# Kernel optimization log

Measured on AMD Instinct MI355X. Metric: run time of the kernel, lower is better.

Reference implementation:

```python
import jax, jax.numpy as jnp
import numpy as np

B, N, INDIM = 512, 200, 200
D1, D2, D3 = 32, 32, 8
RATIO = 0.5
K1 = int(np.ceil(RATIO * N))    # 100 nodes kept after pool1
K2 = int(np.ceil(RATIO * K1))   # 50 nodes kept after pool2
BN_EPS = 1e-5
NEG = -1e9


def setup_inputs() -> dict:
    key = jax.random.key(0)
    ks = jax.random.split(key, 16)
    x = jax.random.normal(ks[0], (B, N, INDIM), jnp.float32)
    u = jax.random.uniform(ks[1], (B, N, N), jnp.float32)
    ut = jnp.triu(jnp.where(u > 0.9, u, 0.0), 1)
    adj = ut + jnp.swapaxes(ut, 1, 2)
    g = lambda i, shape: jax.random.normal(ks[i], shape, jnp.float32) * 0.1
    return dict(
        x=x, adj=adj,
        W1=g(2, (INDIM, D1)), a1s=g(3, (D1,)), a1d=g(4, (D1,)), b1=jnp.zeros((D1,), jnp.float32),
        W2=g(5, (D1, D2)), a2s=g(6, (D2,)), a2d=g(7, (D2,)), b2=jnp.zeros((D2,), jnp.float32),
        pw1=g(8, (D1,)), pw2=g(9, (D2,)),
        fc1_w=g(10, ((D1 + D2) * 2, D2)), fc1_b=jnp.zeros((D2,), jnp.float32),
        fc2_w=g(11, (D2, D3)), fc2_b=jnp.zeros((D3,), jnp.float32),
        fc3_w=g(12, (D3, 2)), fc3_b=jnp.zeros((2,), jnp.float32),
        bn4_g=jnp.ones((D2,), jnp.float32), bn4_b=jnp.zeros((D2,), jnp.float32),
        bn5_g=jnp.ones((D3,), jnp.float32), bn5_b=jnp.zeros((D3,), jnp.float32))


def _gat(x, mask, W, a_s, a_d, b):
    # PyG GATConv (heads=1): alpha_ij = softmax_j LeakyReLU(a_d.h_i + a_s.h_j) over in-neighbors j (self-loops added)
    h = jnp.einsum('bnf,fd->bnd', x, W)
    es = h @ a_s                    # [B,n] source term
    ed = h @ a_d                    # [B,n] dest term
    m = mask | jnp.eye(mask.shape[1], dtype=bool)
    logits = jax.nn.leaky_relu(ed[:, :, None] + es[:, None, :], 0.2)
    alpha = jax.nn.softmax(jnp.where(m, logits, NEG), axis=-1)   # [B,n,n]
    return jnp.einsum('bij,bjd->bid', alpha, h) + b


def _topk(x, adj_w, w, k):
    # TopKPooling(multiplier=1, nonlinearity=sigmoid): score = sigmoid(x.w/||w||)
    score = jax.nn.sigmoid((x @ w) / (jnp.linalg.norm(w) + 1e-16))   # [B,n]
    vals, idx = jax.lax.top_k(score, k)                              # perm sorted desc, as PyG
    xk = jnp.take_along_axis(x, idx[:, :, None], axis=1) * vals[:, :, None]
    ak = jnp.take_along_axis(jnp.take_along_axis(adj_w, idx[:, :, None], axis=1), idx[:, None, :], axis=2)
    return xk, ak, vals


def _bn(z, g, b):
    # eval-mode BatchNorm1d: running_mean=0, running_var=1
    return g * z / jnp.sqrt(1.0 + BN_EPS) + b


def reference(x, adj, W1, a1s, a1d, b1, W2, a2s, a2d, b2, pw1, pw2,
              fc1_w, fc1_b, fc2_w, fc2_b, fc3_w, fc3_b, bn4_g, bn4_b, bn5_g, bn5_b):
    h = _gat(x, adj > 0, W1, a1s, a1d, b1)
    h, aw, s1 = _topk(h, adj, pw1, K1)
    x1 = jnp.concatenate([h.max(axis=1), h.mean(axis=1)], axis=1)    # [B, 64]
    # augment_adj: add self-loops, spspmm (A+I)@(A+I), remove self-loops
    eye = jnp.eye(K1, dtype=aw.dtype)
    a2 = jnp.einsum('bij,bjk->bik', aw + eye, aw + eye) * (1.0 - eye)
    h = _gat(h, a2 != 0, W2, a2s, a2d, b2)
    h, _, s2 = _topk(h, a2, pw2, K2)
    x2 = jnp.concatenate([h.max(axis=1), h.mean(axis=1)], axis=1)    # [B, 64]
    z = jnp.concatenate([x1, x2], axis=1)                            # [B, 128]
    z = _bn(jax.nn.relu(z @ fc1_w + fc1_b), bn4_g, bn4_b)            # dropout: eval -> identity
    z = _bn(jax.nn.relu(z @ fc2_w + fc2_b), bn5_g, bn5_b)
    logp = jax.nn.log_softmax(z @ fc3_w + fc3_b, axis=-1)            # [B, 2]
    return logp, s1, s2
```

## Files before the change

kernel.cpp:

```cpp
#include <hip/hip_runtime.h>
#include <math.h>

#define N_    200
#define B_    512
#define K1_   100
#define K2_   50
#define ST    36
#define XS    21
#define KT    20
#define NT    10

#define S1_OFF 1024
#define S2_OFF 52224

__device__ __forceinline__ float lrelu(float v) { return v > 0.f ? v : 0.2f * v; }
__device__ __forceinline__ float sigm(float v)  { return 1.f / (1.f + __expf(-v)); }


__global__ __launch_bounds__(256) void gnn_fused(
    const float* __restrict__ x, const float* __restrict__ adj,
    const float* __restrict__ W1, const float* __restrict__ a1s,
    const float* __restrict__ a1d, const float* __restrict__ b1,
    const float* __restrict__ W2g, const float* __restrict__ a2s,
    const float* __restrict__ a2d, const float* __restrict__ b2,
    const float* __restrict__ pw1, const float* __restrict__ pw2,
    const float* __restrict__ fc1w, const float* __restrict__ fc1b,
    const float* __restrict__ fc2w, const float* __restrict__ fc2b,
    const float* __restrict__ fc3w, const float* __restrict__ fc3b,
    const float* __restrict__ bn4g, const float* __restrict__ bn4b,
    const float* __restrict__ bn5g, const float* __restrict__ bn5b,
    float* __restrict__ out)
{
  __shared__ __align__(16) char smem[72768];
  float*    sXs   = (float*)smem;
  float*    sW2   = (float*)smem;
  unsigned* sMask2= (unsigned*)(smem + 4096);
  float*    sH    = (float*)(smem + 33600);
  float*    sXK   = sH + 100 * ST;
  unsigned* sBITS = (unsigned*)(smem + 62400);
  float*    sES   = (float*)(smem + 68800);
  float*    sED   = (float*)(smem + 69600);
  float*    sKey  = (float*)(smem + 70400);
  int*      sSel  = (int*)(smem + 71424);
  float*    sVal  = (float*)(smem + 71824);
  float*    sXV   = (float*)(smem + 72224);
  float*    sRed  = (float*)(smem + 72736);

  const int t  = threadIdx.x;
  const int b  = blockIdx.x;
  const int wv = t >> 6, ln = t & 63;
  const float* xb = x   + (size_t)b * N_ * N_;
  const float* ab = adj + (size_t)b * N_ * N_;
  const float4* xb4 = (const float4*)xb;

  float acc[32];
  #pragma unroll
  for (int d = 0; d < 32; ++d) acc[d] = 0.f;

  float4 q0, q1, q2, q3;
  {
    int f0 = t,        r0 = f0 / 5, c0 = f0 % 5;
    int f1 = t + 256,  r1 = f1 / 5, c1 = f1 % 5;
    int f2 = t + 512,  r2 = f2 / 5, c2 = f2 % 5;
    int f3 = t + 768,  r3 = f3 / 5, c3 = f3 % 5;
    q0 = xb4[r0 * 50 + c0];
    q1 = xb4[r1 * 50 + c1];
    q2 = xb4[r2 * 50 + c2];
    if (f3 < 1000) q3 = xb4[r3 * 50 + c3];
    float* d0 = sXs + r0 * XS + c0 * 4; d0[0]=q0.x; d0[1]=q0.y; d0[2]=q0.z; d0[3]=q0.w;
    float* d1 = sXs + r1 * XS + c1 * 4; d1[0]=q1.x; d1[1]=q1.y; d1[2]=q1.z; d1[3]=q1.w;
    float* d2 = sXs + r2 * XS + c2 * 4; d2[0]=q2.x; d2[1]=q2.y; d2[2]=q2.z; d2[3]=q2.w;
    if (f3 < 1000) { float* d3 = sXs + r3 * XS + c3 * 4; d3[0]=q3.x; d3[1]=q3.y; d3[2]=q3.z; d3[3]=q3.w; }
  }
  __syncthreads();

  int cur = 0;
  for (int it = 0; it < NT; ++it) {
    if (it + 1 < NT) {
      int kb4 = (it + 1) * (KT / 4);
      int f0 = t,       r0 = f0 / 5, c0 = f0 % 5;
      int f1 = t + 256, r1 = f1 / 5, c1 = f1 % 5;
      int f2 = t + 512, r2 = f2 / 5, c2 = f2 % 5;
      int f3 = t + 768, r3 = f3 / 5, c3 = f3 % 5;
      q0 = xb4[r0 * 50 + kb4 + c0];
      q1 = xb4[r1 * 50 + kb4 + c1];
      q2 = xb4[r2 * 50 + kb4 + c2];
      if (f3 < 1000) q3 = xb4[r3 * 50 + kb4 + c3];
    }
    {
      int rbase = wv * 50 + it * 5;
      for (int rr = 0; rr < 5; ++rr) {
        int row = rbase + rr;
        const float* arow = ab + row * N_;
        float a0 = arow[ln];
        float a1 = arow[64 + ln];
        float a2 = arow[128 + ln];
        float a3 = (ln < 8) ? arow[192 + ln] : -1.f;
        unsigned long long b0 = __ballot(a0 > 0.f);
        unsigned long long b1 = __ballot(a1 > 0.f);
        unsigned long long b2 = __ballot(a2 > 0.f);
        unsigned long long b3 = __ballot(a3 > 0.f);
        if (ln == 0) {
          sBITS[row * 8 + 0] = (unsigned)b0; sBITS[row * 8 + 1] = (unsigned)(b0 >> 32);
          sBITS[row * 8 + 2] = (unsigned)b1; sBITS[row * 8 + 3] = (unsigned)(b1 >> 32);
          sBITS[row * 8 + 4] = (unsigned)b2; sBITS[row * 8 + 5] = (unsigned)(b2 >> 32);
          sBITS[row * 8 + 6] = (unsigned)b3;
        }
      }
    }
    if (t < N_) {
      const float* xr = sXs + cur * 4200 + t * XS;
      const int k0 = it * KT;
      for (int k = 0; k < KT; k += 4) {
        float x0 = xr[k], x1 = xr[k + 1], x2 = xr[k + 2], x3 = xr[k + 3];
        const float* w0 = W1 + (k0 + k) * 32;
        const float* w1 = w0 + 32;
        const float* w2 = w0 + 64;
        const float* w3 = w0 + 96;
        #pragma unroll
        for (int d = 0; d < 32; ++d) acc[d] += x0 * w0[d];
        #pragma unroll
        for (int d = 0; d < 32; ++d) acc[d] += x1 * w1[d];
        #pragma unroll
        for (int d = 0; d < 32; ++d) acc[d] += x2 * w2[d];
        #pragma unroll
        for (int d = 0; d < 32; ++d) acc[d] += x3 * w3[d];
      }
    }
    __syncthreads();
    if (it + 1 < NT) {
      float* B = sXs + (cur ^ 1) * 4200;
      int f0 = t,       r0 = f0 / 5, c0 = f0 % 5;
      int f1 = t + 256, r1 = f1 / 5, c1 = f1 % 5;
      int f2 = t + 512, r2 = f2 / 5, c2 = f2 % 5;
      int f3 = t + 768, r3 = f3 / 5, c3 = f3 % 5;
      float* d0 = B + r0 * XS + c0 * 4; d0[0]=q0.x; d0[1]=q0.y; d0[2]=q0.z; d0[3]=q0.w;
      float* d1 = B + r1 * XS + c1 * 4; d1[0]=q1.x; d1[1]=q1.y; d1[2]=q1.z; d1[3]=q1.w;
      float* d2 = B + r2 * XS + c2 * 4; d2[0]=q2.x; d2[1]=q2.y; d2[2]=q2.z; d2[3]=q2.w;
      if (f3 < 1000) { float* d3 = B + r3 * XS + c3 * 4; d3[0]=q3.x; d3[1]=q3.y; d3[2]=q3.z; d3[3]=q3.w; }
      __syncthreads();
    }
    cur ^= 1;
  }

  if (t < N_) {
    float es = 0.f, ed = 0.f;
    #pragma unroll
    for (int d = 0; d < 32; ++d) { es += acc[d] * a1s[d]; ed += acc[d] * a1d[d]; }
    sES[t] = es; sED[t] = ed;
    #pragma unroll
    for (int d = 0; d < 32; ++d) sH[t * ST + d] = acc[d];
  }
  __syncthreads();

  for (int i = t; i < 1024; i += 256) sW2[i] = W2g[i];
  {
    float v = (t < N_) ? sES[t] : -3.0e38f;
    #pragma unroll
    for (int off = 1; off < 64; off <<= 1) v = fmaxf(v, __shfl_xor(v, off, 64));
    if ((t & 63) == 0) sRed[t >> 6] = v;
  }
  __syncthreads();
  {
    float esmax = fmaxf(fmaxf(sRed[0], sRed[1]), fmaxf(sRed[2], sRed[3]));

    if (t < N_) {
      unsigned long long m0 = (unsigned long long)sBITS[t * 8 + 0] | ((unsigned long long)sBITS[t * 8 + 1] << 32);
      unsigned long long m1 = (unsigned long long)sBITS[t * 8 + 2] | ((unsigned long long)sBITS[t * 8 + 3] << 32);
      unsigned long long m2 = (unsigned long long)sBITS[t * 8 + 4] | ((unsigned long long)sBITS[t * 8 + 5] << 32);
      unsigned long long m3 = (unsigned long long)sBITS[t * 8 + 6];
      if (t < 64)       m0 |= 1ull << t;
      else if (t < 128) m1 |= 1ull << (t - 64);
      else if (t < 192) m2 |= 1ull << (t - 128);
      else              m3 |= 1ull << (t - 192);
      float ed_i = sED[t];
      float L = lrelu(ed_i + esmax);
      float ssum = 0.f;
      #pragma unroll
      for (int d = 0; d < 32; ++d) acc[d] = 0.f;
      #define AGG(mm, base)                                                        \
        while (mm) {                                                               \
          int j = (base) + (int)__builtin_ctzll(mm); mm &= (mm - 1);               \
          float w = __expf(lrelu(ed_i + sES[j]) - L); ssum += w;                   \
          const float* hr = &sH[j * ST];                                           \
          _Pragma("unroll")                                                        \
          for (int c = 0; c < 8; ++c) {                                            \
            float4 hv = *(const float4*)(hr + c * 4);                              \
            acc[c*4+0] += w * hv.x; acc[c*4+1] += w * hv.y;                        \
            acc[c*4+2] += w * hv.z; acc[c*4+3] += w * hv.w;                        \
          }                                                                        \
        }
      AGG(m0, 0) AGG(m1, 64) AGG(m2, 128) AGG(m3, 192)
      #undef AGG
      float inv = 1.f / ssum;
      #pragma unroll
      for (int d = 0; d < 32; ++d) acc[d] = acc[d] * inv + b1[d];
    }
    __syncthreads();
    if (t < N_) {
      #pragma unroll
      for (int d = 0; d < 32; ++d) sH[t * ST + d] = acc[d];
    }
  }
  __syncthreads();

  {
    float npw = 0.f;
    #pragma unroll
    for (int d = 0; d < 32; ++d) npw += pw1[d] * pw1[d];
    npw = sqrtf(npw) + 1e-16f;
    float sc = -1.f;
    if (t < N_) {
      float dp = 0.f;
      #pragma unroll
      for (int d = 0; d < 32; ++d) dp += sH[t * ST + d] * pw1[d];
      sc = sigm(dp / npw);
    }
    sKey[t] = sc;
  }
  __syncthreads();
  if (t < N_) {
    float sc = sKey[t];
    int rank = 0;
    for (int j = 0; j < N_; j += 4) {
      #pragma unroll
      for (int jj = 0; jj < 4; ++jj) {
        float o = sKey[j + jj];
        rank += (o > sc || (o == sc && (j + jj) < t)) ? 1 : 0;
      }
    }
    if (rank < K1_) {
      sSel[rank] = t; sVal[rank] = sc;
      out[S1_OFF + b * K1_ + rank] = sc;
    }
  }
  __syncthreads();
  {
    float tmp[13];
    #pragma unroll
    for (int it = 0; it < 13; ++it) {
      int i = t + it * 256;
      if (i < K1_ * 32) tmp[it] = sH[sSel[i >> 5] * ST + (i & 31)] * sVal[i >> 5];
    }
    __syncthreads();
    #pragma unroll
    for (int it = 0; it < 13; ++it) {
      int i = t + it * 256;
      if (i < K1_ * 32) sXK[(i >> 5) * ST + (i & 31)] = tmp[it];
    }
  }
  __syncthreads();
  if (t < 32) {
    float m = -3.0e38f, s = 0.f;
    for (int r = 0; r < K1_; ++r) { float v = sXK[r * ST + t]; m = fmaxf(m, v); s += v; }
    sXV[t] = m; sXV[32 + t] = s / 100.f;
  }

  if (t < K1_) {
    int gi = sSel[t];
    #pragma unroll
    for (int w = 0; w < 4; ++w) {
      unsigned m = 0;
      const int lim = (w < 3) ? 32 : 4;
      for (int jj = 0; jj < lim; ++jj) {
        int j = w * 32 + jj;
        int gj = sSel[j];
        unsigned bit = (sBITS[gi * 8 + (gj >> 5)] >> (gj & 31)) & 1u;
        if (j == t) bit = 1u;
        m |= bit << jj;
      }
      sMask2[t * 5 + w] = m;
    }
  }
  __syncthreads();
  {
    unsigned pr0 = 0, pr1 = 0, pr2 = 0, pr3 = 0;
    if (t < K1_) {
      #pragma unroll
      for (int kw = 0; kw < 4; ++kw) {
        unsigned mk = sMask2[t * 5 + kw];
        const int lim = (kw < 3) ? 32 : 4;
        for (int kk = 0; kk < lim; ++kk) {
          if ((mk >> kk) & 1u) {
            int k = kw * 32 + kk;
            pr0 |= sMask2[k * 5 + 0]; pr1 |= sMask2[k * 5 + 1];
            pr2 |= sMask2[k * 5 + 2]; pr3 |= sMask2[k * 5 + 3];
          }
        }
      }
    }
    __syncthreads();
    if (t < K1_) {
      sMask2[t * 5 + 0] = pr0; sMask2[t * 5 + 1] = pr1;
      sMask2[t * 5 + 2] = pr2; sMask2[t * 5 + 3] = pr3;
    }
  }
  __syncthreads();

  if (t < K1_) {
    float xk[32];
    #pragma unroll
    for (int c = 0; c < 8; ++c) *(float4*)&xk[c * 4] = *(const float4*)&sXK[t * ST + c * 4];
    float acc2[32];
    #pragma unroll
    for (int d = 0; d < 32; ++d) acc2[d] = 0.f;
    #pragma unroll
    for (int k = 0; k < 32; ++k) {
      float xv = xk[k];
      const float* wr = &sW2[k * 32];
      #pragma unroll
      for (int d = 0; d < 32; ++d) acc2[d] += xv * wr[d];
    }
    float es = 0.f, ed = 0.f;
    #pragma unroll
    for (int d = 0; d < 32; ++d) { es += acc2[d] * a2s[d]; ed += acc2[d] * a2d[d]; }
    sES[t] = es; sED[t] = ed;
    #pragma unroll
    for (int d = 0; d < 32; ++d) sH[t * ST + d] = acc2[d];
  }
  __syncthreads();
  {
    float v = (t < K1_) ? sES[t] : -3.0e38f;
    #pragma unroll
    for (int off = 1; off < 64; off <<= 1) v = fmaxf(v, __shfl_xor(v, off, 64));
    if ((t & 63) == 0) sRed[t >> 6] = v;
  }
  __syncthreads();
  {
    float esm2 = fmaxf(fmaxf(sRed[0], sRed[1]), fmaxf(sRed[2], sRed[3]));
    float acc2[32];
    if (t < K1_) {
      float ed_i = sED[t];
      float L = lrelu(ed_i + esm2);
      float ssum = 0.f;
      #pragma unroll
      for (int d = 0; d < 32; ++d) acc2[d] = 0.f;
      #pragma unroll
      for (int jw = 0; jw < 4; ++jw) {
        unsigned mw = sMask2[t * 5 + jw];
        const int lim = (jw < 3) ? 32 : 4;
        for (int jj = 0; jj < lim; ++jj) {
          int j = jw * 32 + jj;
          float w = 0.f;
          if ((mw >> jj) & 1u) w = __expf(lrelu(ed_i + sES[j]) - L);
          ssum += w;
          const float* hr = &sH[j * ST];
          #pragma unroll
          for (int d = 0; d < 32; ++d) acc2[d] += w * hr[d];
        }
      }
      float inv = 1.f / ssum;
      #pragma unroll
      for (int d = 0; d < 32; ++d) acc2[d] = acc2[d] * inv + b2[d];
    }
    __syncthreads();
    if (t < K1_) {
      #pragma unroll
      for (int d = 0; d < 32; ++d) sH[t * ST + d] = acc2[d];
    }
  }
  __syncthreads();

  {
    float npw = 0.f;
    #pragma unroll
    for (int d = 0; d < 32; ++d) npw += pw2[d] * pw2[d];
    npw = sqrtf(npw) + 1e-16f;
    if (t < K1_) {
      float dp = 0.f;
      #pragma unroll
      for (int d = 0; d < 32; ++d) dp += sH[t * ST + d] * pw2[d];
      sKey[t] = sigm(dp / npw);
    }
  }
  __syncthreads();
  if (t < K1_) {
    float sc = sKey[t];
    int rank = 0;
    for (int j = 0; j < K1_; j += 4) {
      #pragma unroll
      for (int jj = 0; jj < 4; ++jj) {
        float o = sKey[j + jj];
        rank += (o > sc || (o == sc && (j + jj) < t)) ? 1 : 0;
      }
    }
    if (rank < K2_) {
      sSel[rank] = t; sVal[rank] = sc;
      out[S2_OFF + b * K2_ + rank] = sc;
    }
  }
  __syncthreads();
  {
    int d = t & 31, r0 = t >> 5;
    for (int r = r0; r < K2_; r += 8) sXK[r * ST + d] = sH[sSel[r] * ST + d] * sVal[r];
  }
  __syncthreads();
  if (t < 32) {
    float m = -3.0e38f, s = 0.f;
    for (int r = 0; r < K2_; ++r) { float v = sXK[r * ST + t]; m = fmaxf(m, v); s += v; }
    sXV[64 + t] = m; sXV[96 + t] = s / 50.f;
  }
  __syncthreads();

  const float RS = 0.99999500003749969f;
  if (t < 32) {
    float z = fc1b[t];
    for (int k = 0; k < 128; ++k) z += sXV[k] * fc1w[k * 32 + t];
    z = fmaxf(z, 0.f);
    z = bn4g[t] * z * RS + bn4b[t];
    sKey[t] = z;
  }
  __syncthreads();
  if (t < 8) {
    float z = fc2b[t];
    for (int k = 0; k < 32; ++k) z += sKey[k] * fc2w[k * 8 + t];
    z = fmaxf(z, 0.f);
    z = bn5g[t] * z * RS + bn5b[t];
    sKey[32 + t] = z;
  }
  __syncthreads();
  if (t < 2) {
    float z = fc3b[t];
    for (int k = 0; k < 8; ++k) z += sKey[32 + k] * fc3w[k * 2 + t];
    sKey[40 + t] = z;
  }
  __syncthreads();
  if (t < 2) {
    float z0 = sKey[40], z1 = sKey[41];
    float m = fmaxf(z0, z1);
    float lse = m + logf(__expf(z0 - m) + __expf(z1 - m));
    out[b * 2 + t] = sKey[40 + t] - lse;
  }
}

extern "C" void kernel_launch(void* const* d_in, const int* in_sizes, int n_in,
                              void* d_out, int out_size, void* d_ws, size_t ws_size,
                              hipStream_t stream) {
  (void)in_sizes; (void)n_in; (void)d_ws; (void)ws_size; (void)out_size;
  const float* x    = (const float*)d_in[0];
  const float* adj  = (const float*)d_in[1];
  const float* W1   = (const float*)d_in[2];
  const float* a1s  = (const float*)d_in[3];
  const float* a1d  = (const float*)d_in[4];
  const float* b1   = (const float*)d_in[5];
  const float* W2   = (const float*)d_in[6];
  const float* a2s  = (const float*)d_in[7];
  const float* a2d  = (const float*)d_in[8];
  const float* b2   = (const float*)d_in[9];
  const float* pw1  = (const float*)d_in[10];
  const float* pw2  = (const float*)d_in[11];
  const float* fc1w = (const float*)d_in[12];
  const float* fc1b = (const float*)d_in[13];
  const float* fc2w = (const float*)d_in[14];
  const float* fc2b = (const float*)d_in[15];
  const float* fc3w = (const float*)d_in[16];
  const float* fc3b = (const float*)d_in[17];
  const float* bn4g = (const float*)d_in[18];
  const float* bn4b = (const float*)d_in[19];
  const float* bn5g = (const float*)d_in[20];
  const float* bn5b = (const float*)d_in[21];

  gnn_fused<<<B_, 256, 0, stream>>>(x, adj, W1, a1s, a1d, b1, W2, a2s, a2d, b2,
                                    pw1, pw2, fc1w, fc1b, fc2w, fc2b, fc3w, fc3b,
                                    bn4g, bn4b, bn5g, bn5b, (float*)d_out);
}
```

Baseline: 343.7 us.

## Split fused kernel into parallel projection/mask kernel and graph kernel

The first GAT projection (x@W1) and the adjacency-to-bitmask conversion move out of the single per-graph kernel into a separate kernel with four blocks per graph. That kernel splits nodes and output columns across blocks and waves and writes h and the mask bits to the workspace. The second kernel reloads them and runs the rest of the pipeline with a smaller shared-memory footprint, so more blocks fit per CU. The aim is more parallelism and occupancy for the memory-heavy first stage, at the cost of a global round trip for h and bits plus an extra launch.

```diff
diff --git a/kernel.cpp b/kernel.cpp
--- a/kernel.cpp
+++ b/kernel.cpp
@@ -6,23 +6,76 @@
 #define K1_   100
 #define K2_   50
 #define ST    36
-#define XS    21
-#define KT    20
-#define NT    10
 
 #define S1_OFF 1024
 #define S2_OFF 52224
 
+#define WS_BITS_OFF 13107200
+
 __device__ __forceinline__ float lrelu(float v) { return v > 0.f ? v : 0.2f * v; }
 __device__ __forceinline__ float sigm(float v)  { return 1.f / (1.f + __expf(-v)); }
 
-
-__global__ __launch_bounds__(256) void gnn_fused(
+__global__ __launch_bounds__(256) void gnn_k1(
     const float* __restrict__ x, const float* __restrict__ adj,
-    const float* __restrict__ W1, const float* __restrict__ a1s,
-    const float* __restrict__ a1d, const float* __restrict__ b1,
-    const float* __restrict__ W2g, const float* __restrict__ a2s,
-    const float* __restrict__ a2d, const float* __restrict__ b2,
+    const float* __restrict__ W1, float* __restrict__ gh,
+    unsigned* __restrict__ gbits)
+{
+  const int bid = blockIdx.x;
+  const int g = bid >> 2, c = bid & 3;
+  const int t = threadIdx.x;
+  const int wv = t >> 6, ln = t & 63;
+  const float* ag = adj + (size_t)g * N_ * N_;
+
+  for (int r = wv; r < 50; r += 4) {
+    int row = c * 50 + r;
+    const float* arow = ag + row * N_;
+    float a0 = arow[ln];
+    float a1 = arow[64 + ln];
+    float a2 = arow[128 + ln];
+    float a3 = (ln < 8) ? arow[192 + ln] : -1.f;
+    unsigned long long b0 = __ballot(a0 > 0.f);
+    unsigned long long b1 = __ballot(a1 > 0.f);
+    unsigned long long b2 = __ballot(a2 > 0.f);
+    unsigned long long b3 = __ballot(a3 > 0.f);
+    if (ln == 0) {
+      unsigned* bp = gbits + (size_t)(g * N_ + row) * 8;
+      *(uint4*)bp       = make_uint4((unsigned)b0, (unsigned)(b0 >> 32),
+                                     (unsigned)b1, (unsigned)(b1 >> 32));
+      *(uint4*)(bp + 4) = make_uint4((unsigned)b2, (unsigned)(b2 >> 32),
+                                     (unsigned)b3, 0u);
+    }
+  }
+
+  const int q = wv, n = t & 63;
+  if (n < 50) {
+    const int node = c * 50 + n;
+    const float* xr = x + (size_t)g * N_ * N_ + node * N_;
+    const float* Wq = W1 + q * 8;
+    float acc[8];
+    #pragma unroll
+    for (int d = 0; d < 8; ++d) acc[d] = 0.f;
+    for (int k = 0; k < N_; k += 4) {
+      float4 xv = *(const float4*)(xr + k);
+      #pragma unroll
+      for (int kk = 0; kk < 4; ++kk) {
+        float xs = (&xv.x)[kk];
+        const float* wr = Wq + (k + kk) * 32;
+        #pragma unroll
+        for (int d = 0; d < 8; ++d) acc[d] += xs * wr[d];
+      }
+    }
+    float* hp = gh + (size_t)(g * N_ + node) * 32 + q * 8;
+    *(float4*)hp       = make_float4(acc[0], acc[1], acc[2], acc[3]);
+    *(float4*)(hp + 4) = make_float4(acc[4], acc[5], acc[6], acc[7]);
+  }
+}
+
+__global__ __launch_bounds__(256) void gnn_k2(
+    const float* __restrict__ gh, const unsigned* __restrict__ gbits,
+    const float* __restrict__ a1s, const float* __restrict__ a1d,
+    const float* __restrict__ b1,  const float* __restrict__ W2g,
+    const float* __restrict__ a2s, const float* __restrict__ a2d,
+    const float* __restrict__ b2,
     const float* __restrict__ pw1, const float* __restrict__ pw2,
     const float* __restrict__ fc1w, const float* __restrict__ fc1b,
     const float* __restrict__ fc2w, const float* __restrict__ fc2b,
@@ -31,129 +84,56 @@
     const float* __restrict__ bn5g, const float* __restrict__ bn5b,
     float* __restrict__ out)
 {
-  __shared__ __align__(16) char smem[72768];
-  float*    sXs   = (float*)smem;
-  float*    sW2   = (float*)smem;
-  unsigned* sMask2= (unsigned*)(smem + 4096);
-  float*    sH    = (float*)(smem + 33600);
+  __shared__ __align__(16) char smem[45264];
+  float*    sH    = (float*)smem;
   float*    sXK   = sH + 100 * ST;
-  unsigned* sBITS = (unsigned*)(smem + 62400);
-  float*    sES   = (float*)(smem + 68800);
-  float*    sED   = (float*)(smem + 69600);
-  float*    sKey  = (float*)(smem + 70400);
-  int*      sSel  = (int*)(smem + 71424);
-  float*    sVal  = (float*)(smem + 71824);
-  float*    sXV   = (float*)(smem + 72224);
-  float*    sRed  = (float*)(smem + 72736);
-
-  const int t  = threadIdx.x;
-  const int b  = blockIdx.x;
-  const int wv = t >> 6, ln = t & 63;
-  const float* xb = x   + (size_t)b * N_ * N_;
-  const float* ab = adj + (size_t)b * N_ * N_;
-  const float4* xb4 = (const float4*)xb;
-
-  float acc[32];
-  #pragma unroll
-  for (int d = 0; d < 32; ++d) acc[d] = 0.f;
-
-  float4 q0, q1, q2, q3;
-  {
-    int f0 = t,        r0 = f0 / 5, c0 = f0 % 5;
-    int f1 = t + 256,  r1 = f1 / 5, c1 = f1 % 5;
-    int f2 = t + 512,  r2 = f2 / 5, c2 = f2 % 5;
-    int f3 = t + 768,  r3 = f3 / 5, c3 = f3 % 5;
-    q0 = xb4[r0 * 50 + c0];
-    q1 = xb4[r1 * 50 + c1];
-    q2 = xb4[r2 * 50 + c2];
-    if (f3 < 1000) q3 = xb4[r3 * 50 + c3];
-    float* d0 = sXs + r0 * XS + c0 * 4; d0[0]=q0.x; d0[1]=q0.y; d0[2]=q0.z; d0[3]=q0.w;
-    float* d1 = sXs + r1 * XS + c1 * 4; d1[0]=q1.x; d1[1]=q1.y; d1[2]=q1.z; d1[3]=q1.w;
-    float* d2 = sXs + r2 * XS + c2 * 4; d2[0]=q2.x; d2[1]=q2.y; d2[2]=q2.z; d2[3]=q2.w;
-    if (f3 < 1000) { float* d3 = sXs + r3 * XS + c3 * 4; d3[0]=q3.x; d3[1]=q3.y; d3[2]=q3.z; d3[3]=q3.w; }
-  }
-  __syncthreads();
-
-  int cur = 0;
-  for (int it = 0; it < NT; ++it) {
-    if (it + 1 < NT) {
-      int kb4 = (it + 1) * (KT / 4);
-      int f0 = t,       r0 = f0 / 5, c0 = f0 % 5;
-      int f1 = t + 256, r1 = f1 / 5, c1 = f1 % 5;
-      int f2 = t + 512, r2 = f2 / 5, c2 = f2 % 5;
-      int f3 = t + 768, r3 = f3 / 5, c3 = f3 % 5;
-      q0 = xb4[r0 * 50 + kb4 + c0];
-      q1 = xb4[r1 * 50 + kb4 + c1];
-      q2 = xb4[r2 * 50 + kb4 + c2];
-      if (f3 < 1000) q3 = xb4[r3 * 50 + kb4 + c3];
-    }
-    {
-      int rbase = wv * 50 + it * 5;
-      for (int rr = 0; rr < 5; ++rr) {
-        int row = rbase + rr;
-        const float* arow = ab + row * N_;
-        float a0 = arow[ln];
-        float a1 = arow[64 + ln];
-        float a2 = arow[128 + ln];
-        float a3 = (ln < 8) ? arow[192 + ln] : -1.f;
-        unsigned long long b0 = __ballot(a0 > 0.f);
-        unsigned long long b1 = __ballot(a1 > 0.f);
-        unsigned long long b2 = __ballot(a2 > 0.f);
-        unsigned long long b3 = __ballot(a3 > 0.f);
-        if (ln == 0) {
-          sBITS[row * 8 + 0] = (unsigned)b0; sBITS[row * 8 + 1] = (unsigned)(b0 >> 32);
-          sBITS[row * 8 + 2] = (unsigned)b1; sBITS[row * 8 + 3] = (unsigned)(b1 >> 32);
-          sBITS[row * 8 + 4] = (unsigned)b2; sBITS[row * 8 + 5] = (unsigned)(b2 >> 32);
-          sBITS[row * 8 + 6] = (unsigned)b3;
-        }
-      }
-    }
-    if (t < N_) {
-      const float* xr = sXs + cur * 4200 + t * XS;
-      const int k0 = it * KT;
-      for (int k = 0; k < KT; k += 4) {
-        float x0 = xr[k], x1 = xr[k + 1], x2 = xr[k + 2], x3 = xr[k + 3];
-        const float* w0 = W1 + (k0 + k) * 32;
-        const float* w1 = w0 + 32;
-        const float* w2 = w0 + 64;
-        const float* w3 = w0 + 96;
-        #pragma unroll
-        for (int d = 0; d < 32; ++d) acc[d] += x0 * w0[d];
-        #pragma unroll
-        for (int d = 0; d < 32; ++d) acc[d] += x1 * w1[d];
-        #pragma unroll
-        for (int d = 0; d < 32; ++d) acc[d] += x2 * w2[d];
-        #pragma unroll
-        for (int d = 0; d < 32; ++d) acc[d] += x3 * w3[d];
-      }
-    }
-    __syncthreads();
-    if (it + 1 < NT) {
-      float* B = sXs + (cur ^ 1) * 4200;
-      int f0 = t,       r0 = f0 / 5, c0 = f0 % 5;
-      int f1 = t + 256, r1 = f1 / 5, c1 = f1 % 5;
-      int f2 = t + 512, r2 = f2 / 5, c2 = f2 % 5;
-      int f3 = t + 768, r3 = f3 / 5, c3 = f3 % 5;
-      float* d0 = B + r0 * XS + c0 * 4; d0[0]=q0.x; d0[1]=q0.y; d0[2]=q0.z; d0[3]=q0.w;
-      float* d1 = B + r1 * XS + c1 * 4; d1[0]=q1.x; d1[1]=q1.y; d1[2]=q1.z; d1[3]=q1.w;
-      float* d2 = B + r2 * XS + c2 * 4; d2[0]=q2.x; d2[1]=q2.y; d2[2]=q2.z; d2[3]=q2.w;
-      if (f3 < 1000) { float* d3 = B + r3 * XS + c3 * 4; d3[0]=q3.x; d3[1]=q3.y; d3[2]=q3.z; d3[3]=q3.w; }
-      __syncthreads();
-    }
-    cur ^= 1;
-  }
+  unsigned* sBITS = (unsigned*)(smem + 28800);
+  float*    sW2   = (float*)(smem + 35200);
+  unsigned* sMask2= (unsigned*)(smem + 39296);
+  float*    sES   = (float*)(smem + 41296);
+  float*    sED   = (float*)(smem + 42096);
+  float*    sKey  = (float*)(smem + 42896);
+  int*      sSel  = (int*)(smem + 43920);
+  float*    sVal  = (float*)(smem + 44320);
+  float*    sXV   = (float*)(smem + 44720);
+  float*    sRed  = (float*)(smem + 45232);
+
+  const int t = threadIdx.x;
+  const int b = blockIdx.x;
+
+  {
+    const float4* src = (const float4*)(gh + (size_t)b * N_ * 32);
+    #pragma unroll
+    for (int i = 0; i < 7; ++i) {
+      int j = t + i * 256;
+      if (j < 1600) {
+        float4 v = src[j];
+        int node = j >> 3, c4 = j & 7;
+        *(float4*)&sH[node * ST + c4 * 4] = v;
+      }
+    }
+    const unsigned* bsrc = gbits + (size_t)b * N_ * 8;
+    #pragma unroll
+    for (int i = 0; i < 7; ++i) {
+      int j = t + i * 256;
+      if (j < 1600) sBITS[j] = bsrc[j];
+    }
+    for (int i = t; i < 1024; i += 256) sW2[i] = W2g[i];
+  }
+  __syncthreads();
 
   if (t < N_) {
     float es = 0.f, ed = 0.f;
     #pragma unroll
-    for (int d = 0; d < 32; ++d) { es += acc[d] * a1s[d]; ed += acc[d] * a1d[d]; }
+    for (int c = 0; c < 8; ++c) {
+      float4 hv = *(const float4*)&sH[t * ST + c * 4];
+      es += hv.x * a1s[c*4+0] + hv.y * a1s[c*4+1] + hv.z * a1s[c*4+2] + hv.w * a1s[c*4+3];
+      ed += hv.x * a1d[c*4+0] + hv.y * a1d[c*4+1] + hv.z * a1d[c*4+2] + hv.w * a1d[c*4+3];
+    }
     sES[t] = es; sED[t] = ed;
-    #pragma unroll
-    for (int d = 0; d < 32; ++d) sH[t * ST + d] = acc[d];
-  }
-  __syncthreads();
-
-  for (int i = t; i < 1024; i += 256) sW2[i] = W2g[i];
+  }
+  __syncthreads();
+
   {
     float v = (t < N_) ? sES[t] : -3.0e38f;
     #pragma unroll
@@ -164,6 +144,7 @@
   {
     float esmax = fmaxf(fmaxf(sRed[0], sRed[1]), fmaxf(sRed[2], sRed[3]));
 
+    float acc[32];
     if (t < N_) {
       unsigned long long m0 = (unsigned long long)sBITS[t * 8 + 0] | ((unsigned long long)sBITS[t * 8 + 1] << 32);
       unsigned long long m1 = (unsigned long long)sBITS[t * 8 + 2] | ((unsigned long long)sBITS[t * 8 + 3] << 32);
@@ -436,7 +417,7 @@
 extern "C" void kernel_launch(void* const* d_in, const int* in_sizes, int n_in,
                               void* d_out, int out_size, void* d_ws, size_t ws_size,
                               hipStream_t stream) {
-  (void)in_sizes; (void)n_in; (void)d_ws; (void)ws_size; (void)out_size;
+  (void)in_sizes; (void)n_in; (void)ws_size; (void)out_size;
   const float* x    = (const float*)d_in[0];
   const float* adj  = (const float*)d_in[1];
   const float* W1   = (const float*)d_in[2];
@@ -460,7 +441,11 @@
   const float* bn5g = (const float*)d_in[20];
   const float* bn5b = (const float*)d_in[21];
 
-  gnn_fused<<<B_, 256, 0, stream>>>(x, adj, W1, a1s, a1d, b1, W2, a2s, a2d, b2,
-                                    pw1, pw2, fc1w, fc1b, fc2w, fc2b, fc3w, fc3b,
-                                    bn4g, bn4b, bn5g, bn5b, (float*)d_out);
+  float*    gh    = (float*)d_ws;
+  unsigned* gbits = (unsigned*)((char*)d_ws + WS_BITS_OFF);
+
+  gnn_k1<<<B_ * 4, 256, 0, stream>>>(x, adj, W1, gh, gbits);
+  gnn_k2<<<B_, 256, 0, stream>>>(gh, gbits, a1s, a1d, b1, W2, a2s, a2d, b2,
+                                 pw1, pw2, fc1w, fc1b, fc2w, fc2b, fc3w, fc3b,
+                                 bn4g, bn4b, bn5g, bn5b, (float*)d_out);
 }
```

Measured after the change: 400.2 us. 16.4% more time.
